# Kernel tuning notes

Measured on AMD Instinct MI355X. Metric: run time of the kernel, lower is better.

## Reference

```python
import jax, jax.numpy as jnp
import numpy as np

N_LAYERS = 4
N_QUBITS = 2
BATCH = 1_048_576

_I2 = jnp.eye(2, dtype=jnp.complex64)
_X2 = jnp.array([[0.0, 1.0], [1.0, 0.0]], dtype=jnp.complex64)


def _rx_batch(theta):
    """Batched RX(theta): (B,) -> (B,2,2) complex64. RX = cos(t/2) I - i sin(t/2) X."""
    c = jnp.cos(theta * 0.5)
    s = jnp.sin(theta * 0.5)
    return c[:, None, None] * _I2 - 1j * s[:, None, None] * _X2


def _rot(phi, theta, omega):
    """PennyLane Rot(phi, theta, omega) = RZ(omega) RY(theta) RZ(phi), 2x2 complex."""
    c = jnp.cos(theta * 0.5)
    s = jnp.sin(theta * 0.5)
    ep = jnp.exp(-0.5j * (phi + omega))  # e^{-i(phi+omega)/2}
    em = jnp.exp(-0.5j * (phi - omega))  # e^{-i(phi-omega)/2}
    return jnp.stack([
        jnp.stack([ep * c, -jnp.conj(em) * s]),
        jnp.stack([em * s, jnp.conj(ep) * c]),
    ]).astype(jnp.complex64)


def _quantum(inputs, weights):
    """Simulate the 2-qubit re-uploading circuit for a batch of inputs.

    inputs: (B, 2) float angles; weights: (N_LAYERS, 2, 3) float.
    State is stored as (B, 2, 2) complex64 indexed [batch, qubit0, qubit1].
    Returns (B, 2): [<Z0>, <Z1>].
    """
    B = inputs.shape[0]
    state = jnp.zeros((B, 2, 2), dtype=jnp.complex64).at[:, 0, 0].set(1.0)
    U0 = _rx_batch(inputs[:, 0])  # per-sample RX on wire 0
    U1 = _rx_batch(inputs[:, 1])  # per-sample RX on wire 1
    for l in range(N_LAYERS):
        # AngleEmbedding (default rotation='X'): RX(x0) wire0, RX(x1) wire1
        state = jnp.einsum('bij,bjk->bik', U0, state)
        state = jnp.einsum('bij,bkj->bki', U1, state)
        # StronglyEntanglingLayers, one layer: Rot on each wire (shared weights)
        R0 = _rot(weights[l, 0, 0], weights[l, 0, 1], weights[l, 0, 2])
        R1 = _rot(weights[l, 1, 0], weights[l, 1, 1], weights[l, 1, 2])
        state = jnp.einsum('ij,bjk->bik', R0, state)
        state = jnp.einsum('ij,bkj->bki', R1, state)
        # ring of CNOTs with range 1 on 2 wires: CNOT(0,1) then CNOT(1,0)
        state = jnp.stack([state[:, 0, :], state[:, 1, ::-1]], axis=1)  # CNOT(0,1)
        state = jnp.stack([state[:, :, 0], state[:, ::-1, 1]], axis=2)  # CNOT(1,0)
    p = state.real ** 2 + state.imag ** 2  # (B,2,2) probabilities
    z0 = p[:, 0, :].sum(-1) - p[:, 1, :].sum(-1)
    z1 = p[:, :, 0].sum(-1) - p[:, :, 1].sum(-1)
    return jnp.stack([z0, z1], axis=-1)


def setup_inputs() -> dict:
    key = jax.random.key(0)
    ks = jax.random.split(key, 8)
    return {
        'x': jax.random.normal(ks[0], (BATCH, 2), dtype=jnp.float32),
        'pre_w1': jax.random.normal(ks[1], (4, 2), dtype=jnp.float32) * 0.5,
        'pre_b1': jax.random.normal(ks[2], (4,), dtype=jnp.float32) * 0.1,
        'pre_w2': jax.random.normal(ks[3], (2, 4), dtype=jnp.float32) * 0.5,
        'pre_b2': jax.random.normal(ks[4], (2,), dtype=jnp.float32) * 0.1,
        'q_weights': jax.random.uniform(ks[5], (N_LAYERS, N_QUBITS, 3), dtype=jnp.float32,
                                        minval=0.0, maxval=2.0 * np.pi),
        'post_w': jax.random.normal(ks[6], (1, 2), dtype=jnp.float32) * 0.5,
        'post_b': jax.random.normal(ks[7], (1,), dtype=jnp.float32) * 0.1,
    }


def reference(x, pre_w1, pre_b1, pre_w2, pre_b2, q_weights, post_w, post_b):
    # classical pre: Linear(2->4)+Tanh, Linear(4->2)+Tanh
    h = jnp.tanh(x @ pre_w1.T + pre_b1)
    h = jnp.tanh(h @ pre_w2.T + pre_b2)
    # quantum layer: two PauliZ expectations in [-1, 1]
    q = _quantum(h, q_weights)
    q = (q + 1.0) * 0.5
    # classical post: Linear(2->1) + Sigmoid
    return jax.nn.sigmoid(q @ post_w.T + post_b)
```

## Files before the change

### kernel.cpp

```cpp
#include <hip/hip_runtime.h>


#define TN 256

struct c2 { float re, im; };

__device__ __forceinline__ c2 cmul(c2 a, c2 b) {
    c2 r;
    r.re = fmaf(a.re, b.re, -(a.im * b.im));
    r.im = fmaf(a.re, b.im, a.im * b.re);
    return r;
}

__device__ __forceinline__ c2 cfma(c2 a, c2 b, c2 acc) {
    acc.re = fmaf(a.re, b.re, fmaf(-a.im, b.im, acc.re));
    acc.im = fmaf(a.re, b.im, fmaf(a.im, b.re, acc.im));
    return acc;
}

__device__ __forceinline__ void rx_pair(c2& u, c2& v, float c, float s) {
    c2 nu, nv;
    nu.re = fmaf(c, u.re,  s * v.im);
    nu.im = fmaf(c, u.im, -(s * v.re));
    nv.re = fmaf(c, v.re,  s * u.im);
    nv.im = fmaf(c, v.im, -(s * u.re));
    u = nu; v = nv;
}

__device__ __forceinline__ void rot_pair(c2& u, c2& v, c2 g00, c2 g01, c2 g10, c2 g11) {
    c2 nu = cmul(g00, u); nu = cfma(g01, v, nu);
    c2 nv = cmul(g10, u); nv = cfma(g11, v, nv);
    u = nu; v = nv;
}

__device__ __forceinline__ float ftanh(float v) {
    float e = __expf(2.0f * v);
    return __fdividef(e - 1.0f, e + 1.0f);
}

__device__ __forceinline__ void u_bounds(const float* w2, const float* b2,
                                         float& B0, float& B1) {
    B0 = fabsf(w2[0]) + fabsf(w2[1]) + fabsf(w2[2]) + fabsf(w2[3]) + fabsf(b2[0]);
    B1 = fabsf(w2[4]) + fabsf(w2[5]) + fabsf(w2[6]) + fabsf(w2[7]) + fabsf(b2[1]);
}

__device__ __forceinline__ float circuit_y(float g0, float g1,
                                           const float (*Rs)[2][8],
                                           float pw0, float pw1, float pb) {
    float cs0 = __cosf(0.5f * g0), sn0 = __sinf(0.5f * g0);
    float cs1 = __cosf(0.5f * g1), sn1 = __sinf(0.5f * g1);

    c2 s00 = {1.0f, 0.0f}, s01 = {0.0f, 0.0f};
    c2 s10 = {0.0f, 0.0f}, s11 = {0.0f, 0.0f};

#pragma unroll
    for (int l = 0; l < 4; l++) {
        rx_pair(s00, s10, cs0, sn0);
        rx_pair(s01, s11, cs0, sn0);
        rx_pair(s00, s01, cs1, sn1);
        rx_pair(s10, s11, cs1, sn1);
        {
            const float* r = Rs[l][0];
            c2 g00 = {r[0], r[1]}, g01 = {r[2], r[3]};
            c2 g10 = {r[4], r[5]}, g11 = {r[6], r[7]};
            rot_pair(s00, s10, g00, g01, g10, g11);
            rot_pair(s01, s11, g00, g01, g10, g11);
        }
        {
            const float* r = Rs[l][1];
            c2 g00 = {r[0], r[1]}, g01 = {r[2], r[3]};
            c2 g10 = {r[4], r[5]}, g11 = {r[6], r[7]};
            rot_pair(s00, s01, g00, g01, g10, g11);
            rot_pair(s10, s11, g00, g01, g10, g11);
        }
        { c2 tmp = s10; s10 = s11; s11 = tmp; }
        { c2 tmp = s01; s01 = s11; s11 = tmp; }
    }

    float p00 = fmaf(s00.re, s00.re, s00.im * s00.im);
    float p01 = fmaf(s01.re, s01.re, s01.im * s01.im);
    float p10 = fmaf(s10.re, s10.re, s10.im * s10.im);
    float p11 = fmaf(s11.re, s11.re, s11.im * s11.im);
    float z0 = (p00 + p01) - (p10 + p11);
    float z1 = (p00 + p10) - (p01 + p11);

    float q0 = 0.5f * (z0 + 1.0f);
    float q1 = 0.5f * (z1 + 1.0f);
    float y  = fmaf(pw0, q0, fmaf(pw1, q1, pb));
    return __fdividef(1.0f, 1.0f + __expf(-y));
}

__global__ __launch_bounds__(256) void build_table(
    const float* __restrict__ qw,
    const float* __restrict__ pre_w2,
    const float* __restrict__ pre_b2,
    const float* __restrict__ post_w,
    const float* __restrict__ post_b,
    float* __restrict__ table)
{
    __shared__ float Rs[4][2][8];
    int tid = threadIdx.x;
    if (tid < 8) {
        int l = tid >> 1, w = tid & 1;
        const float* p = qw + (l * 2 + w) * 3;
        float phi = p[0], th = p[1], om = p[2];
        float c  = cosf(0.5f * th), s = sinf(0.5f * th);
        float a  = 0.5f * (phi + om), b = 0.5f * (phi - om);
        float ca = cosf(a), sa = sinf(a);
        float cb = cosf(b), sb = sinf(b);
        float* r = Rs[l][w];
        r[0] =  c * ca;  r[1] = -c * sa;
        r[2] = -s * cb;  r[3] = -s * sb;
        r[4] =  s * cb;  r[5] = -s * sb;
        r[6] =  c * ca;  r[7] =  c * sa;
    }
    __syncthreads();

    int k = blockIdx.x * 256 + tid;
    int i = k & (TN - 1);
    int j = k >> 8;

    float B0, B1;
    u_bounds(pre_w2, pre_b2, B0, B1);

    float u0 = fmaf((2.0f * B0) / (float)(TN - 1), (float)i, -B0);
    float u1 = fmaf((2.0f * B1) / (float)(TN - 1), (float)j, -B1);
    float g0 = ftanh(u0);
    float g1 = ftanh(u1);

    table[k] = circuit_y(g0, g1, Rs, post_w[0], post_w[1], post_b[0]);
}

__global__ __launch_bounds__(256) void eval_kernel(
    const float* __restrict__ x,
    const float* __restrict__ pre_w1,
    const float* __restrict__ pre_b1,
    const float* __restrict__ pre_w2,
    const float* __restrict__ pre_b2,
    const float* __restrict__ table,
    float* __restrict__ out,
    int nbatch)
{
    float w1[8], b1[4], w2[8], b2[2];
#pragma unroll
    for (int i = 0; i < 8; i++) w1[i] = pre_w1[i];
#pragma unroll
    for (int i = 0; i < 4; i++) b1[i] = pre_b1[i];
#pragma unroll
    for (int i = 0; i < 8; i++) w2[i] = pre_w2[i];
#pragma unroll
    for (int i = 0; i < 2; i++) b2[i] = pre_b2[i];

    float B0, B1;
    u_bounds(w2, b2, B0, B1);
    float sc0 = (float)(TN - 1) / (2.0f * B0);
    float sc1 = (float)(TN - 1) / (2.0f * B1);

    int base = (blockIdx.x * blockDim.x + threadIdx.x) * 2;
    if (base >= nbatch) return;

    float4 xin = *reinterpret_cast<const float4*>(x + 2 * (long long)base);
    float xs0[2] = { xin.x, xin.z };
    float xs1[2] = { xin.y, xin.w };
    float res[2];

#pragma unroll
    for (int t = 0; t < 2; t++) {
        float x0 = xs0[t], x1 = xs1[t];

        float h0 = ftanh(fmaf(w1[0], x0, fmaf(w1[1], x1, b1[0])));
        float h1 = ftanh(fmaf(w1[2], x0, fmaf(w1[3], x1, b1[1])));
        float h2 = ftanh(fmaf(w1[4], x0, fmaf(w1[5], x1, b1[2])));
        float h3 = ftanh(fmaf(w1[6], x0, fmaf(w1[7], x1, b1[3])));

        float u0 = fmaf(w2[0], h0, fmaf(w2[1], h1, fmaf(w2[2], h2, fmaf(w2[3], h3, b2[0]))));
        float u1 = fmaf(w2[4], h0, fmaf(w2[5], h1, fmaf(w2[6], h2, fmaf(w2[7], h3, b2[1]))));

        float t0 = (u0 + B0) * sc0;
        float t1 = (u1 + B1) * sc1;
        t0 = fminf(fmaxf(t0, 0.0f), (float)(TN - 1));
        t1 = fminf(fmaxf(t1, 0.0f), (float)(TN - 1));
        float i0f = fminf(floorf(t0), (float)(TN - 2));
        float j0f = fminf(floorf(t1), (float)(TN - 2));
        float f0 = t0 - i0f;
        float f1 = t1 - j0f;
        int i0 = (int)i0f;
        int j0 = (int)j0f;

        const float* p = table + j0 * TN + i0;
        float a = p[0], b = p[1], c = p[TN], d = p[TN + 1];
        float top = fmaf(f0, b - a, a);
        float bot = fmaf(f0, d - c, c);
        res[t] = fmaf(f1, bot - top, top);
    }

    *reinterpret_cast<float2*>(out + base) = make_float2(res[0], res[1]);
}

extern "C" void kernel_launch(void* const* d_in, const int* in_sizes, int n_in,
                              void* d_out, int out_size, void* d_ws, size_t ws_size,
                              hipStream_t stream) {
    const float* x      = (const float*)d_in[0];
    const float* pre_w1 = (const float*)d_in[1];
    const float* pre_b1 = (const float*)d_in[2];
    const float* pre_w2 = (const float*)d_in[3];
    const float* pre_b2 = (const float*)d_in[4];
    const float* qw     = (const float*)d_in[5];
    const float* post_w = (const float*)d_in[6];
    const float* post_b = (const float*)d_in[7];
    float* out   = (float*)d_out;
    float* table = (float*)d_ws;

    hipLaunchKernelGGL(build_table, dim3((TN * TN) / 256), dim3(256), 0, stream,
                       qw, pre_w2, pre_b2, post_w, post_b, table);

    int nbatch  = in_sizes[0] / 2;
    int threads = 256;
    int spb     = threads * 2;
    int blocks  = (nbatch + spb - 1) / spb;
    hipLaunchKernelGGL(eval_kernel, dim3(blocks), dim3(threads), 0, stream,
                       x, pre_w1, pre_b1, pre_w2, pre_b2, table, out, nbatch);
}
```

Before: 78.87 us.

## Fuse table build and evaluation into one cooperative kernel with grid sync

Merges the lookup-table build kernel and the batch evaluation kernel into a single cooperative launch of a fixed 1024 blocks. The first 256 blocks fill the table, then a grid-wide barrier lets every block read it. Each thread now handles four samples with float4 loads and stores instead of two. This removes a second kernel launch and its gap, at the cost of a grid barrier, a fixed grid size that must exactly cover the batch, and cooperative-launch overhead.

Result: slower. 194.9 us (+147.1%).

```diff
diff --git a/kernel.cpp b/kernel.cpp
--- a/kernel.cpp
+++ b/kernel.cpp
@@ -1,7 +1,12 @@
 #include <hip/hip_runtime.h>
+#include <hip/hip_cooperative_groups.h>
+
+namespace cg = cooperative_groups;
 
 
 #define TN 256
+#define NBLOCKS 1024
+#define NTHREADS 256
 
 struct c2 { float re, im; };
 
@@ -90,57 +95,54 @@
     return __fdividef(1.0f, 1.0f + __expf(-y));
 }
 
-__global__ __launch_bounds__(256) void build_table(
-    const float* __restrict__ qw,
-    const float* __restrict__ pre_w2,
-    const float* __restrict__ pre_b2,
-    const float* __restrict__ post_w,
-    const float* __restrict__ post_b,
-    float* __restrict__ table)
-{
-    __shared__ float Rs[4][2][8];
-    int tid = threadIdx.x;
-    if (tid < 8) {
-        int l = tid >> 1, w = tid & 1;
-        const float* p = qw + (l * 2 + w) * 3;
-        float phi = p[0], th = p[1], om = p[2];
-        float c  = cosf(0.5f * th), s = sinf(0.5f * th);
-        float a  = 0.5f * (phi + om), b = 0.5f * (phi - om);
-        float ca = cosf(a), sa = sinf(a);
-        float cb = cosf(b), sb = sinf(b);
-        float* r = Rs[l][w];
-        r[0] =  c * ca;  r[1] = -c * sa;
-        r[2] = -s * cb;  r[3] = -s * sb;
-        r[4] =  s * cb;  r[5] = -s * sb;
-        r[6] =  c * ca;  r[7] =  c * sa;
-    }
-    __syncthreads();
-
-    int k = blockIdx.x * 256 + tid;
-    int i = k & (TN - 1);
-    int j = k >> 8;
-
-    float B0, B1;
-    u_bounds(pre_w2, pre_b2, B0, B1);
-
-    float u0 = fmaf((2.0f * B0) / (float)(TN - 1), (float)i, -B0);
-    float u1 = fmaf((2.0f * B1) / (float)(TN - 1), (float)j, -B1);
-    float g0 = ftanh(u0);
-    float g1 = ftanh(u1);
-
-    table[k] = circuit_y(g0, g1, Rs, post_w[0], post_w[1], post_b[0]);
-}
-
-__global__ __launch_bounds__(256) void eval_kernel(
+__global__ __launch_bounds__(NTHREADS, 4) void fused_kernel(
     const float* __restrict__ x,
     const float* __restrict__ pre_w1,
     const float* __restrict__ pre_b1,
     const float* __restrict__ pre_w2,
     const float* __restrict__ pre_b2,
-    const float* __restrict__ table,
+    const float* __restrict__ qw,
+    const float* __restrict__ post_w,
+    const float* __restrict__ post_b,
+    float* __restrict__ table,
     float* __restrict__ out,
     int nbatch)
 {
+    int tid = threadIdx.x;
+    int bid = blockIdx.x;
+
+    float B0, B1;
+    u_bounds(pre_w2, pre_b2, B0, B1);
+
+    if (bid < (TN * TN) / NTHREADS) {
+        __shared__ float Rs[4][2][8];
+        if (tid < 8) {
+            int l = tid >> 1, w = tid & 1;
+            const float* p = qw + (l * 2 + w) * 3;
+            float phi = p[0], th = p[1], om = p[2];
+            float c  = cosf(0.5f * th), s = sinf(0.5f * th);
+            float a  = 0.5f * (phi + om), b = 0.5f * (phi - om);
+            float ca = cosf(a), sa = sinf(a);
+            float cb = cosf(b), sb = sinf(b);
+            float* r = Rs[l][w];
+            r[0] =  c * ca;  r[1] = -c * sa;
+            r[2] = -s * cb;  r[3] = -s * sb;
+            r[4] =  s * cb;  r[5] = -s * sb;
+            r[6] =  c * ca;  r[7] =  c * sa;
+        }
+        __syncthreads();
+
+        int k = bid * NTHREADS + tid;
+        int i = k & (TN - 1);
+        int j = k >> 8;
+        float u0 = fmaf((2.0f * B0) / (float)(TN - 1), (float)i, -B0);
+        float u1 = fmaf((2.0f * B1) / (float)(TN - 1), (float)j, -B1);
+        table[k] = circuit_y(ftanh(u0), ftanh(u1), Rs,
+                             post_w[0], post_w[1], post_b[0]);
+    }
+
+    cg::this_grid().sync();
+
     float w1[8], b1[4], w2[8], b2[2];
 #pragma unroll
     for (int i = 0; i < 8; i++) w1[i] = pre_w1[i];
@@ -151,21 +153,20 @@
 #pragma unroll
     for (int i = 0; i < 2; i++) b2[i] = pre_b2[i];
 
-    float B0, B1;
-    u_bounds(w2, b2, B0, B1);
     float sc0 = (float)(TN - 1) / (2.0f * B0);
     float sc1 = (float)(TN - 1) / (2.0f * B1);
 
-    int base = (blockIdx.x * blockDim.x + threadIdx.x) * 2;
+    int base = (bid * NTHREADS + tid) * 4;
     if (base >= nbatch) return;
 
-    float4 xin = *reinterpret_cast<const float4*>(x + 2 * (long long)base);
-    float xs0[2] = { xin.x, xin.z };
-    float xs1[2] = { xin.y, xin.w };
-    float res[2];
-
-#pragma unroll
-    for (int t = 0; t < 2; t++) {
+    float4 xa = *reinterpret_cast<const float4*>(x + 2 * (long long)base);
+    float4 xb = *reinterpret_cast<const float4*>(x + 2 * (long long)base + 4);
+    float xs0[4] = { xa.x, xa.z, xb.x, xb.z };
+    float xs1[4] = { xa.y, xa.w, xb.y, xb.w };
+    float res[4];
+
+#pragma unroll
+    for (int t = 0; t < 4; t++) {
         float x0 = xs0[t], x1 = xs1[t];
 
         float h0 = ftanh(fmaf(w1[0], x0, fmaf(w1[1], x1, b1[0])));
@@ -194,7 +195,7 @@
         res[t] = fmaf(f1, bot - top, top);
     }
 
-    *reinterpret_cast<float2*>(out + base) = make_float2(res[0], res[1]);
+    *reinterpret_cast<float4*>(out + base) = make_float4(res[0], res[1], res[2], res[3]);
 }
 
 extern "C" void kernel_launch(void* const* d_in, const int* in_sizes, int n_in,
@@ -210,14 +211,14 @@
     const float* post_b = (const float*)d_in[7];
     float* out   = (float*)d_out;
     float* table = (float*)d_ws;
-
-    hipLaunchKernelGGL(build_table, dim3((TN * TN) / 256), dim3(256), 0, stream,
-                       qw, pre_w2, pre_b2, post_w, post_b, table);
-
-    int nbatch  = in_sizes[0] / 2;
-    int threads = 256;
-    int spb     = threads * 2;
-    int blocks  = (nbatch + spb - 1) / spb;
-    hipLaunchKernelGGL(eval_kernel, dim3(blocks), dim3(threads), 0, stream,
-                       x, pre_w1, pre_b1, pre_w2, pre_b2, table, out, nbatch);
-}
+    int nbatch   = in_sizes[0] / 2;
+
+    void* args[] = {
+        (void*)&x, (void*)&pre_w1, (void*)&pre_b1, (void*)&pre_w2, (void*)&pre_b2,
+        (void*)&qw, (void*)&post_w, (void*)&post_b, (void*)&table, (void*)&out,
+        (void*)&nbatch,
+    };
+    hipLaunchCooperativeKernel((const void*)fused_kernel,
+                               dim3(NBLOCKS), dim3(NTHREADS),
+                               args, 0, stream);
+}
```
